# Optimization experiments

Measured on AMD Instinct MI355X. Metric: run time of the kernel, lower is better.

The kernel has to match this reference:

```python
import jax, jax.numpy as jnp
import numpy as np

B, S, D, H = 4, 4096, 256, 4
Dh = D // H


def setup_inputs() -> dict:
    key = jax.random.key(0)
    ks = jax.random.split(key, 5)
    scale = 1.0 / np.sqrt(D)
    return {
        "inputs": jax.random.normal(ks[0], (B, S, D), dtype=jnp.float32),
        "Wq": jax.random.normal(ks[1], (D, D), dtype=jnp.float32) * scale,
        "bq": jnp.zeros((D,), jnp.float32),
        "Wk": jax.random.normal(ks[2], (D, D), dtype=jnp.float32) * scale,
        "bk": jnp.zeros((D,), jnp.float32),
        "Wv": jax.random.normal(ks[3], (D, D), dtype=jnp.float32) * scale,
        "bv": jnp.zeros((D,), jnp.float32),
        "Wo": jax.random.normal(ks[4], (D, D), dtype=jnp.float32) * scale,
        "bo": jnp.zeros((D,), jnp.float32),
    }


def reference(inputs, Wq, bq, Wk, bk, Wv, bv, Wo, bo):
    b, s, d = inputs.shape
    # QKV projections
    q = inputs @ Wq + bq
    k = inputs @ Wk + bk
    v = inputs @ Wv + bv
    # separate heads: [B, S, D] -> [B, H, S, Dh]
    def split_heads(x):
        return x.reshape(b, s, H, Dh).transpose(0, 2, 1, 3)
    q, k, v = split_heads(q), split_heads(k), split_heads(v)
    # scaled dot-product attention (no causal mask: mask=False)
    scores = jnp.einsum("bhqd,bhkd->bhqk", q, k) / jnp.sqrt(jnp.float32(Dh))
    weights = jax.nn.softmax(scores, axis=-1)
    attn = jnp.einsum("bhqk,bhkd->bhqd", weights, v)
    # combine heads: [B, H, S, Dh] -> [B, S, D]
    attn = attn.transpose(0, 2, 1, 3).reshape(b, s, d)
    return attn @ Wo + bo
```

## Files before the change

### kernel.cpp

```cpp
#include <hip/hip_runtime.h>
#include <cmath>

#define B_  4
#define S_  4096
#define D_  256
#define H_  4
#define DH_ 64
#define M_TOTAL (B_*S_)
#define QSCALE 0.1803368801111f

typedef __bf16 bf16x8 __attribute__((ext_vector_type(8)));
typedef __bf16 bf16x4 __attribute__((ext_vector_type(4)));
typedef __bf16 bf16x2 __attribute__((ext_vector_type(2)));
typedef float  f32x4  __attribute__((ext_vector_type(4)));
typedef float  f32x16 __attribute__((ext_vector_type(16)));

#define AS1 __attribute__((address_space(1)))
#define AS3 __attribute__((address_space(3)))

__device__ __forceinline__ void g2lds16(const void* g, void* l) {
    __builtin_amdgcn_global_load_lds((AS1 const void*)g, (AS3 void*)l, 16, 0, 0);
}

#if __has_builtin(__builtin_amdgcn_permlane32_swap)
typedef unsigned uint2v __attribute__((ext_vector_type(2)));
__device__ __forceinline__ void plswap(unsigned &a, unsigned &b) {
    uint2v r = __builtin_amdgcn_permlane32_swap(a, b, false, false);
    a = r[0]; b = r[1];
}
#else
__device__ __forceinline__ void plswap(unsigned &a, unsigned &b) {
    unsigned bl = (unsigned)__shfl_xor((int)b, 32);
    unsigned ah = (unsigned)__shfl_xor((int)a, 32);
    bool hi = (threadIdx.x & 32) != 0;
    unsigned na = hi ? bl : a;
    unsigned nb = hi ? b  : ah;
    a = na; b = nb;
}
#endif

__device__ __forceinline__ unsigned pk2(float x, float y) {
    bf16x2 t; t[0] = (__bf16)x; t[1] = (__bf16)y;
    return __builtin_bit_cast(unsigned, t);
}

__global__ __launch_bounds__(256) void prep(const float* __restrict__ X,
                                            const float* __restrict__ W0,
                                            const float* __restrict__ W1,
                                            const float* __restrict__ W2,
                                            const float* __restrict__ W3,
                                            __bf16* __restrict__ Xb,
                                            __bf16* __restrict__ Wt_all) {
    int t = threadIdx.x;
    if (blockIdx.x < 2048) {
        size_t i = ((size_t)blockIdx.x * 256 + t) * 8;
        float4 v0 = *(const float4*)(X + i);
        float4 v1 = *(const float4*)(X + i + 4);
        bf16x8 o;
        o[0] = (__bf16)v0.x; o[1] = (__bf16)v0.y; o[2] = (__bf16)v0.z; o[3] = (__bf16)v0.w;
        o[4] = (__bf16)v1.x; o[5] = (__bf16)v1.y; o[6] = (__bf16)v1.z; o[7] = (__bf16)v1.w;
        *(bf16x8*)(Xb + i) = o;
        return;
    }
    int bid = blockIdx.x - 2048;
    int z = bid >> 6, rem = bid & 63;
    int by = rem >> 3, bx = rem & 7;
    const float* W = (z == 0) ? W0 : (z == 1) ? W1 : (z == 2) ? W2 : W3;
    float wsc = (z == 0) ? QSCALE : 1.0f;
    __bf16* Wt = Wt_all + (size_t)z * 65536;
    __shared__ float tile[32][33];
    int r0 = by * 32, c0 = bx * 32;
#pragma unroll
    for (int e = 0; e < 4; e++) {
        int idx = t + e * 256; int r = idx >> 5, c = idx & 31;
        tile[r][c] = W[(r0 + r) * 256 + c0 + c];
    }
    __syncthreads();
#pragma unroll
    for (int e = 0; e < 4; e++) {
        int idx = t + e * 256; int r = idx >> 5, c = idx & 31;
        Wt[(c0 + r) * 256 + (r0 + c)] = (__bf16)(tile[c][r] * wsc);
    }
}

__global__ __launch_bounds__(256) void gemm_bt(const __bf16* __restrict__ A,
                                               const __bf16* __restrict__ Wt_all,
                                               const float* __restrict__ bias0,
                                               const float* __restrict__ bias1,
                                               const float* __restrict__ bias2,
                                               __bf16* __restrict__ outb,
                                               __bf16* __restrict__ voutb,
                                               float* __restrict__ outf,
                                               int out_is_f32, float bsc0) {
    constexpr int K = 256;
    __shared__ __attribute__((aligned(16))) __bf16 As[128 * 32];
    __shared__ __attribute__((aligned(16))) __bf16 Bs[128 * 32];

    int t = threadIdx.x;
    int lane = t & 63, w = t >> 6;
    int wr = w >> 1, wc = w & 1;
    int l16 = lane & 15, quad = lane >> 4;
    int mbase = blockIdx.x * 128;
    int nbase = blockIdx.y * 128;
    int z = blockIdx.z;
    const __bf16* Bt = Wt_all + (size_t)z * 65536;
    const float* bias = (z == 0) ? bias0 : (z == 1) ? bias1 : bias2;
    float bscale = (z == 0) ? bsc0 : 1.0f;

    f32x4 acc[4][4] = {};

    int srow = t >> 2;
    int sseg = (t & 3) * 8;

    for (int kk = 0; kk < K; kk += 32) {
        __syncthreads();
        g2lds16(A  + (size_t)(mbase +      srow) * K + kk + sseg, (char*)As +        t * 16);
        g2lds16(A  + (size_t)(mbase + 64 + srow) * K + kk + sseg, (char*)As + 4096 + t * 16);
        g2lds16(Bt + (size_t)(nbase +      srow) * K + kk + sseg, (char*)Bs +        t * 16);
        g2lds16(Bt + (size_t)(nbase + 64 + srow) * K + kk + sseg, (char*)Bs + 4096 + t * 16);
        __syncthreads();

        bf16x8 a[4], b[4];
#pragma unroll
        for (int i = 0; i < 4; i++)
            a[i] = *(const bf16x8*)(As + (wr * 64 + i * 16 + l16) * 32 + quad * 8);
#pragma unroll
        for (int j = 0; j < 4; j++)
            b[j] = *(const bf16x8*)(Bs + (wc * 64 + j * 16 + l16) * 32 + quad * 8);
#pragma unroll
        for (int i = 0; i < 4; i++)
#pragma unroll
            for (int j = 0; j < 4; j++)
                acc[i][j] = __builtin_amdgcn_mfma_f32_16x16x32_bf16(a[i], b[j], acc[i][j], 0, 0, 0);
    }

#pragma unroll
    for (int i = 0; i < 4; i++) {
#pragma unroll
        for (int j = 0; j < 4; j++) {
            int col = nbase + wc * 64 + j * 16 + l16;
            float bv = bias[col] * bscale;
            int row0 = mbase + wr * 64 + i * 16 + quad * 4;
            if (out_is_f32) {
#pragma unroll
                for (int r = 0; r < 4; r++)
                    outf[(size_t)(row0 + r) * 256 + col] = acc[i][j][r] + bv;
            } else if (z == 2) {
                int hcol = col >> 6, dh = col & 63;
                int bidx = row0 >> 12, s0 = row0 & 4095;
                bf16x4 pk;
#pragma unroll
                for (int r = 0; r < 4; r++) pk[r] = (__bf16)(acc[i][j][r] + bv);
                *(bf16x4*)(voutb + ((size_t)(bidx * 4 + hcol) * 64 + dh) * 4096 + s0) = pk;
            } else {
#pragma unroll
                for (int r = 0; r < 4; r++)
                    outb[(size_t)z * ((size_t)M_TOTAL * 256) + (size_t)(row0 + r) * 256 + col] =
                        (__bf16)(acc[i][j][r] + bv);
            }
        }
    }
}

__global__ __launch_bounds__(256, 3) void attn(const __bf16* __restrict__ Qb,
                                               const __bf16* __restrict__ Kb,
                                               const __bf16* __restrict__ Vt,
                                               __bf16* __restrict__ Ctx) {
    __shared__ __attribute__((aligned(16))) __bf16 smem[24576];

    int t = threadIdx.x;
    int lane = t & 63, w = t >> 6;
    int l31 = lane & 31, hh = lane >> 5;
    int kw = w & 1, qw2 = w >> 1;

    int lin = blockIdx.x;
    int xcd = lin & 7, j = lin >> 3;
    int bh = xcd * 2 + (j & 1);
    int qblk = j >> 1;
    int b = bh >> 2, hd = bh & 3;
    int qw = qblk * 128 + qw2 * 64;

    const __bf16* Kbase = Kb + (size_t)b * S_ * 256 + hd * 64;
    const __bf16* Vbase = Vt + (size_t)bh * 64 * S_;

    bf16x8 qf[4][2];
#pragma unroll
    for (int ks = 0; ks < 4; ks++)
#pragma unroll
        for (int qt = 0; qt < 2; qt++)
            qf[ks][qt] = *(const bf16x8*)(Qb + (size_t)(b * S_ + qw + qt * 32 + l31) * 256
                                              + hd * 64 + ks * 16 + hh * 8);

    f32x16 acc[2][2] = {};
    float lsum[2] = {0.f, 0.f};

    int srow = t >> 3;
    int sseg = t & 7;

#define STAGE(kv, slot) do {                                                   \
        char* mk = (char*)smem + (slot) * 16384;                               \
        char* mv = mk + 8192;                                                  \
        _Pragma("unroll")                                                      \
        for (int c = 0; c < 2; c++) {                                          \
            int rr = c * 32 + srow;                                            \
            int gseg = (sseg ^ (rr & 7)) * 8;                                  \
            g2lds16(Kbase + (size_t)((kv) + rr) * 256 + gseg,                  \
                    mk + c * 4096 + t * 16);                                   \
            g2lds16(Vbase + (size_t)rr * S_ + (kv) + gseg,                     \
                    mv + c * 4096 + t * 16);                                   \
        }                                                                      \
    } while (0)

    STAGE(0, 0);
    STAGE(64, 1);

    int rs = 0, ps = 2;
    for (int it = 0; it < 64; it++) {
        if (it < 63) {
            asm volatile("s_waitcnt vmcnt(4)" ::: "memory");
        } else {
            asm volatile("s_waitcnt vmcnt(0)" ::: "memory");
        }
        asm volatile("s_barrier" ::: "memory");
        if (it < 62) STAGE((it + 2) * 64, ps);

        __bf16* Ksp = (__bf16*)((char*)smem + rs * 16384);
        __bf16* Vsp = Ksp + 4096;

        bf16x8 kf[4];
#pragma unroll
        for (int ks = 0; ks < 4; ks++) {
            int slot = (ks * 2 + hh) ^ (l31 & 7);
            kf[ks] = *(const bf16x8*)(Ksp + (kw * 32 + l31) * 64 + slot * 8);
        }
        f32x16 st[2] = {};
#pragma unroll
        for (int ks = 0; ks < 4; ks++)
#pragma unroll
            for (int qt = 0; qt < 2; qt++)
                st[qt] = __builtin_amdgcn_mfma_f32_32x32x16_bf16(kf[ks], qf[ks][qt], st[qt], 0, 0, 0);

        unsigned dd[2][8];
#pragma unroll
        for (int qt = 0; qt < 2; qt++) {
            float p[16];
#pragma unroll
            for (int r = 0; r < 16; r++) p[r] = __builtin_amdgcn_exp2f(st[qt][r]);
            float s0 = ((p[0] + p[1]) + (p[2] + p[3])) + ((p[4] + p[5]) + (p[6] + p[7]));
            float s1 = ((p[8] + p[9]) + (p[10] + p[11])) + ((p[12] + p[13]) + (p[14] + p[15]));
            lsum[qt] += s0 + s1;
#pragma unroll
            for (int m = 0; m < 4; m++) {
                dd[qt][m * 2]     = pk2(p[4 * m],     p[4 * m + 1]);
                dd[qt][m * 2 + 1] = pk2(p[4 * m + 2], p[4 * m + 3]);
            }
        }

#pragma unroll
        for (int tt = 0; tt < 2; tt++) {
            int tks = kw * 2 + tt;
            bf16x8 pf[2];
#pragma unroll
            for (int qt = 0; qt < 2; qt++) {
                unsigned x0 = dd[qt][4 * tt],     y0 = dd[qt][4 * tt + 2];
                unsigned x1 = dd[qt][4 * tt + 1], y1 = dd[qt][4 * tt + 3];
                plswap(x0, y0);
                plswap(x1, y1);
                union { unsigned u[4]; bf16x8 v; } c;
                c.u[0] = x0; c.u[1] = x1; c.u[2] = y0; c.u[3] = y1;
                pf[qt] = c.v;
            }
#pragma unroll
            for (int mt = 0; mt < 2; mt++) {
                int slot = (tks * 2 + hh) ^ (l31 & 7);
                bf16x8 vf = *(const bf16x8*)(Vsp + (mt * 32 + l31) * 64 + slot * 8);
#pragma unroll
                for (int qt = 0; qt < 2; qt++)
                    acc[mt][qt] = __builtin_amdgcn_mfma_f32_32x32x16_bf16(vf, pf[qt], acc[mt][qt], 0, 0, 0);
            }
        }

        rs = (rs == 2) ? 0 : rs + 1;
        ps = (ps == 2) ? 0 : ps + 1;
    }
#undef STAGE

#pragma unroll
    for (int qt = 0; qt < 2; qt++)
        lsum[qt] += __shfl_xor(lsum[qt], 32);

    __syncthreads();
    float* lsd = (float*)((char*)smem + 32768);
    if (kw == 1) {
#pragma unroll
        for (int mt = 0; mt < 2; mt++)
#pragma unroll
            for (int qt = 0; qt < 2; qt++)
#pragma unroll
                for (int g = 0; g < 4; g++) {
                    f32x4 v;
#pragma unroll
                    for (int e = 0; e < 4; e++) v[e] = acc[mt][qt][4 * g + e];
                    *(f32x4*)((char*)smem + qw2 * 16384
                              + ((mt * 2 + qt) * 4 + g) * 1024 + lane * 16) = v;
                }
        lsd[qw2 * 128 + lane * 2 + 0] = lsum[0];
        lsd[qw2 * 128 + lane * 2 + 1] = lsum[1];
    }
    __syncthreads();
    if (kw == 0) {
        float inv[2];
#pragma unroll
        for (int qt = 0; qt < 2; qt++)
            inv[qt] = 1.f / (lsum[qt] + lsd[qw2 * 128 + lane * 2 + qt]);
#pragma unroll
        for (int mt = 0; mt < 2; mt++)
#pragma unroll
            for (int qt = 0; qt < 2; qt++)
#pragma unroll
                for (int g = 0; g < 4; g++) {
                    f32x4 v = *(const f32x4*)((char*)smem + qw2 * 16384
                                              + ((mt * 2 + qt) * 4 + g) * 1024 + lane * 16);
#pragma unroll
                    for (int e = 0; e < 4; e++) acc[mt][qt][4 * g + e] += v[e];
                }
        asm volatile("" ::: "memory");

        __bf16* Es = (__bf16*)((char*)smem + qw2 * 16384);
#pragma unroll
        for (int qt = 0; qt < 2; qt++)
#pragma unroll
            for (int mt = 0; mt < 2; mt++)
#pragma unroll
                for (int rg = 0; rg < 4; rg++) {
                    bf16x4 ov;
#pragma unroll
                    for (int e = 0; e < 4; e++)
                        ov[e] = (__bf16)(acc[mt][qt][4 * rg + e] * inv[qt]);
                    int dhb = mt * 32 + rg * 8 + 4 * hh;
                    *(bf16x4*)(Es + (qt * 32 + l31) * 72 + dhb) = ov;
                }
#pragma unroll
        for (int pass = 0; pass < 8; pass++) {
            int q = pass * 8 + (lane >> 3);
            int col = (lane & 7) * 8;
            bf16x8 val = *(const bf16x8*)(Es + q * 72 + col);
            *(bf16x8*)(Ctx + (size_t)(b * S_ + qw + q) * 256 + hd * 64 + col) = val;
        }
    }
}

extern "C" void kernel_launch(void* const* d_in, const int* in_sizes, int n_in,
                              void* d_out, int out_size, void* d_ws, size_t ws_size,
                              hipStream_t stream) {
    const float* X  = (const float*)d_in[0];
    const float* Wq = (const float*)d_in[1];
    const float* bq = (const float*)d_in[2];
    const float* Wk = (const float*)d_in[3];
    const float* bk = (const float*)d_in[4];
    const float* Wv = (const float*)d_in[5];
    const float* bv = (const float*)d_in[6];
    const float* Wo = (const float*)d_in[7];
    const float* bo = (const float*)d_in[8];
    float* out = (float*)d_out;

    char* ws = (char*)d_ws;
    const size_t MB = 1024 * 1024;
    __bf16* Xb  = (__bf16*)(ws);
    __bf16* Ctx = (__bf16*)(ws);
    __bf16* Wt  = (__bf16*)(ws + 8 * MB);
    __bf16* Qb  = (__bf16*)(ws + 8 * MB + 512 * 1024);
    __bf16* Kb  = (__bf16*)((char*)Qb + 8 * MB);
    __bf16* Vt  = (__bf16*)((char*)Kb + 8 * MB);

    prep<<<dim3(2304), dim3(256), 0, stream>>>(X, Wq, Wk, Wv, Wo, Xb, Wt);
    gemm_bt<<<dim3(M_TOTAL / 128, 2, 3), dim3(256), 0, stream>>>(
        Xb, Wt, bq, bk, bv, Qb, Vt, nullptr, 0, QSCALE);
    attn<<<dim3(512), dim3(256), 0, stream>>>(Qb, Kb, Vt, Ctx);
    gemm_bt<<<dim3(M_TOTAL / 128, 2, 1), dim3(256), 0, stream>>>(
        Ctx, Wt + 3 * 65536, bo, bo, bo, nullptr, nullptr, out, 1, 1.0f);
}
```

Before: 180.3 us.

## Split attention over two KV halves with a separate merge kernel

The attention kernel now splits the key/value sequence into two halves, doubling the grid from 512 to 1024 blocks. Each block writes unnormalized fp32 partial outputs and row sums to workspace. A new merge kernel adds the two partials, normalizes, and writes bf16 context. The aim is better occupancy and load balance on the many-CU GPU, at the cost of an extra launch and roughly 32MB of fp32 partial traffic. The merge appears to rely on the softmax needing no max subtraction, since pre-scaled scores allow plain sums.

```diff
diff --git a/kernel.cpp b/kernel.cpp
--- a/kernel.cpp
+++ b/kernel.cpp
@@ -42,6 +42,12 @@
 __device__ __forceinline__ unsigned pk2(float x, float y) {
     bf16x2 t; t[0] = (__bf16)x; t[1] = (__bf16)y;
     return __builtin_bit_cast(unsigned, t);
+}
+
+__device__ __forceinline__ int part_lin(int bh, int qblk, int ks2) {
+    int xcd = bh >> 1;
+    int j = (ks2 << 6) | (qblk << 1) | (bh & 1);
+    return (j << 3) | xcd;
 }
 
 __global__ __launch_bounds__(256) void prep(const float* __restrict__ X,
@@ -162,10 +168,11 @@
     }
 }
 
-__global__ __launch_bounds__(256, 3) void attn(const __bf16* __restrict__ Qb,
-                                               const __bf16* __restrict__ Kb,
-                                               const __bf16* __restrict__ Vt,
-                                               __bf16* __restrict__ Ctx) {
+__global__ __launch_bounds__(256, 3) void attn_part(const __bf16* __restrict__ Qb,
+                                                    const __bf16* __restrict__ Kb,
+                                                    const __bf16* __restrict__ Vt,
+                                                    float* __restrict__ Opart,
+                                                    float* __restrict__ Lpart) {
     __shared__ __attribute__((aligned(16))) __bf16 smem[24576];
 
     int t = threadIdx.x;
@@ -176,12 +183,13 @@
     int lin = blockIdx.x;
     int xcd = lin & 7, j = lin >> 3;
     int bh = xcd * 2 + (j & 1);
-    int qblk = j >> 1;
+    int qblk = (j >> 1) & 31;
+    int ks2 = j >> 6;
     int b = bh >> 2, hd = bh & 3;
     int qw = qblk * 128 + qw2 * 64;
 
-    const __bf16* Kbase = Kb + (size_t)b * S_ * 256 + hd * 64;
-    const __bf16* Vbase = Vt + (size_t)bh * 64 * S_;
+    const __bf16* Kbase = Kb + (size_t)b * S_ * 256 + hd * 64 + (size_t)ks2 * 2048 * 256;
+    const __bf16* Vbase = Vt + (size_t)bh * 64 * S_ + ks2 * 2048;
 
     bf16x8 qf[4][2];
 #pragma unroll
@@ -215,14 +223,14 @@
     STAGE(64, 1);
 
     int rs = 0, ps = 2;
-    for (int it = 0; it < 64; it++) {
-        if (it < 63) {
+    for (int it = 0; it < 32; it++) {
+        if (it < 31) {
             asm volatile("s_waitcnt vmcnt(4)" ::: "memory");
         } else {
             asm volatile("s_waitcnt vmcnt(0)" ::: "memory");
         }
         asm volatile("s_barrier" ::: "memory");
-        if (it < 62) STAGE((it + 2) * 64, ps);
+        if (it < 30) STAGE((it + 2) * 64, ps);
 
         __bf16* Ksp = (__bf16*)((char*)smem + rs * 16384);
         __bf16* Vsp = Ksp + 4096;
@@ -309,10 +317,11 @@
     }
     __syncthreads();
     if (kw == 0) {
-        float inv[2];
+        float lsc[2];
 #pragma unroll
         for (int qt = 0; qt < 2; qt++)
-            inv[qt] = 1.f / (lsum[qt] + lsd[qw2 * 128 + lane * 2 + qt]);
+            lsc[qt] = lsum[qt] + lsd[qw2 * 128 + lane * 2 + qt];
+        float* Ob = Opart + (size_t)lin * 8192 + qw2 * 4096;
 #pragma unroll
         for (int mt = 0; mt < 2; mt++)
 #pragma unroll
@@ -322,31 +331,74 @@
                     f32x4 v = *(const f32x4*)((char*)smem + qw2 * 16384
                                               + ((mt * 2 + qt) * 4 + g) * 1024 + lane * 16);
 #pragma unroll
-                    for (int e = 0; e < 4; e++) acc[mt][qt][4 * g + e] += v[e];
+                    for (int e = 0; e < 4; e++) v[e] += acc[mt][qt][4 * g + e];
+                    *(f32x4*)(Ob + ((mt * 2 + qt) * 4 + g) * 256 + lane * 4) = v;
                 }
-        asm volatile("" ::: "memory");
-
-        __bf16* Es = (__bf16*)((char*)smem + qw2 * 16384);
+        Lpart[lin * 256 + qw2 * 128 + lane * 2 + 0] = lsc[0];
+        Lpart[lin * 256 + qw2 * 128 + lane * 2 + 1] = lsc[1];
+    }
+}
+
+__global__ __launch_bounds__(256) void attn_merge(const float* __restrict__ Opart,
+                                                  const float* __restrict__ Lpart,
+                                                  __bf16* __restrict__ Ctx) {
+    __shared__ __attribute__((aligned(16))) __bf16 Es_all[4][64 * 72];
+
+    int t = threadIdx.x;
+    int lane = t & 63, w = t >> 6;
+    int l31 = lane & 31, hh = lane >> 5;
+    int id = blockIdx.x * 4 + w;
+    int qw2 = id & 1, qblk = (id >> 1) & 31, bh = id >> 6;
+    int b = bh >> 2, hd = bh & 3;
+    int qw = qblk * 128 + qw2 * 64;
+
+    int lin0 = part_lin(bh, qblk, 0);
+    int lin1 = part_lin(bh, qblk, 1);
+    const float* p0 = Opart + (size_t)lin0 * 8192 + qw2 * 4096;
+    const float* p1 = Opart + (size_t)lin1 * 8192 + qw2 * 4096;
+
+    float inv[2];
+#pragma unroll
+    for (int qt = 0; qt < 2; qt++) {
+        float l0 = Lpart[lin0 * 256 + qw2 * 128 + lane * 2 + qt];
+        float l1 = Lpart[lin1 * 256 + qw2 * 128 + lane * 2 + qt];
+        inv[qt] = 1.f / (l0 + l1);
+    }
+
+    f32x16 acc[2][2];
+#pragma unroll
+    for (int mt = 0; mt < 2; mt++)
 #pragma unroll
         for (int qt = 0; qt < 2; qt++)
 #pragma unroll
-            for (int mt = 0; mt < 2; mt++)
-#pragma unroll
-                for (int rg = 0; rg < 4; rg++) {
-                    bf16x4 ov;
-#pragma unroll
-                    for (int e = 0; e < 4; e++)
-                        ov[e] = (__bf16)(acc[mt][qt][4 * rg + e] * inv[qt]);
-                    int dhb = mt * 32 + rg * 8 + 4 * hh;
-                    *(bf16x4*)(Es + (qt * 32 + l31) * 72 + dhb) = ov;
-                }
-#pragma unroll
-        for (int pass = 0; pass < 8; pass++) {
-            int q = pass * 8 + (lane >> 3);
-            int col = (lane & 7) * 8;
-            bf16x8 val = *(const bf16x8*)(Es + q * 72 + col);
-            *(bf16x8*)(Ctx + (size_t)(b * S_ + qw + q) * 256 + hd * 64 + col) = val;
-        }
+            for (int g = 0; g < 4; g++) {
+                int off = ((mt * 2 + qt) * 4 + g) * 256 + lane * 4;
+                f32x4 v0 = *(const f32x4*)(p0 + off);
+                f32x4 v1 = *(const f32x4*)(p1 + off);
+#pragma unroll
+                for (int e = 0; e < 4; e++) acc[mt][qt][4 * g + e] = v0[e] + v1[e];
+            }
+
+    __bf16* Es = Es_all[w];
+#pragma unroll
+    for (int qt = 0; qt < 2; qt++)
+#pragma unroll
+        for (int mt = 0; mt < 2; mt++)
+#pragma unroll
+            for (int rg = 0; rg < 4; rg++) {
+                bf16x4 ov;
+#pragma unroll
+                for (int e = 0; e < 4; e++)
+                    ov[e] = (__bf16)(acc[mt][qt][4 * rg + e] * inv[qt]);
+                int dhb = mt * 32 + rg * 8 + 4 * hh;
+                *(bf16x4*)(Es + (qt * 32 + l31) * 72 + dhb) = ov;
+            }
+#pragma unroll
+    for (int pass = 0; pass < 8; pass++) {
+        int q = pass * 8 + (lane >> 3);
+        int col = (lane & 7) * 8;
+        bf16x8 val = *(const bf16x8*)(Es + q * 72 + col);
+        *(bf16x8*)(Ctx + (size_t)(b * S_ + qw + q) * 256 + hd * 64 + col) = val;
     }
 }
 
@@ -372,11 +424,14 @@
     __bf16* Qb  = (__bf16*)(ws + 8 * MB + 512 * 1024);
     __bf16* Kb  = (__bf16*)((char*)Qb + 8 * MB);
     __bf16* Vt  = (__bf16*)((char*)Kb + 8 * MB);
+    float*  Opart = (float*)(ws + 33 * MB);
+    float*  Lpart = (float*)(ws + 65 * MB);
 
     prep<<<dim3(2304), dim3(256), 0, stream>>>(X, Wq, Wk, Wv, Wo, Xb, Wt);
     gemm_bt<<<dim3(M_TOTAL / 128, 2, 3), dim3(256), 0, stream>>>(
         Xb, Wt, bq, bk, bv, Qb, Vt, nullptr, 0, QSCALE);
-    attn<<<dim3(512), dim3(256), 0, stream>>>(Qb, Kb, Vt, Ctx);
+    attn_part<<<dim3(1024), dim3(256), 0, stream>>>(Qb, Kb, Vt, Opart, Lpart);
+    attn_merge<<<dim3(256), dim3(256), 0, stream>>>(Opart, Lpart, Ctx);
     gemm_bt<<<dim3(M_TOTAL / 128, 2, 1), dim3(256), 0, stream>>>(
         Ctx, Wt + 3 * 65536, bo, bo, bo, nullptr, nullptr, out, 1, 1.0f);
 }
```

Result: slower. 200.0 us (+10.9%).

## Split attention over key dimension into three partial blocks plus merge kernel

Applied to the files above, without the earlier changes.

Replaces the single attention kernel with a split-K scheme: each block processes one third of the keys (22/21 tiles) for 128 queries, writing fp32 partial outputs and row sums to workspace. A new merge kernel sums the three partials, normalizes, and writes bf16 context. This raises the grid from 512 to 1536 blocks to fill the GPU better and removes the in-block cross-wave LDS reduction. In exchange it adds an extra launch and roughly 48MB of fp32 partial traffic to global memory. Like the original, it relies on exp without max subtraction.

```diff
diff --git a/kernel.cpp b/kernel.cpp
--- a/kernel.cpp
+++ b/kernel.cpp
@@ -42,6 +42,11 @@
 __device__ __forceinline__ unsigned pk2(float x, float y) {
     bf16x2 t; t[0] = (__bf16)x; t[1] = (__bf16)y;
     return __builtin_bit_cast(unsigned, t);
+}
+
+__device__ __forceinline__ int part_lin(int bh, int qblk, int ks3) {
+    int j = (ks3 << 6) | (qblk << 1) | (bh & 1);
+    return (j << 3) | (bh >> 1);
 }
 
 __global__ __launch_bounds__(256) void prep(const float* __restrict__ X,
@@ -162,37 +167,39 @@
     }
 }
 
-__global__ __launch_bounds__(256, 3) void attn(const __bf16* __restrict__ Qb,
-                                               const __bf16* __restrict__ Kb,
-                                               const __bf16* __restrict__ Vt,
-                                               __bf16* __restrict__ Ctx) {
+__global__ __launch_bounds__(256, 3) void attn_part(const __bf16* __restrict__ Qb,
+                                                    const __bf16* __restrict__ Kb,
+                                                    const __bf16* __restrict__ Vt,
+                                                    float* __restrict__ Opart,
+                                                    float* __restrict__ Lpart) {
     __shared__ __attribute__((aligned(16))) __bf16 smem[24576];
 
     int t = threadIdx.x;
     int lane = t & 63, w = t >> 6;
     int l31 = lane & 31, hh = lane >> 5;
-    int kw = w & 1, qw2 = w >> 1;
 
     int lin = blockIdx.x;
     int xcd = lin & 7, j = lin >> 3;
     int bh = xcd * 2 + (j & 1);
-    int qblk = j >> 1;
+    int qblk = (j >> 1) & 31;
+    int ks3 = j >> 6;
     int b = bh >> 2, hd = bh & 3;
-    int qw = qblk * 128 + qw2 * 64;
-
-    const __bf16* Kbase = Kb + (size_t)b * S_ * 256 + hd * 64;
-    const __bf16* Vbase = Vt + (size_t)bh * 64 * S_;
-
-    bf16x8 qf[4][2];
+    int qw = qblk * 128 + w * 32;
+
+    int NT   = ks3 ? 21 : 22;
+    int key0 = ks3 ? (1408 + (ks3 - 1) * 1344) : 0;
+
+    const __bf16* Kbase = Kb + (size_t)b * S_ * 256 + hd * 64 + (size_t)key0 * 256;
+    const __bf16* Vbase = Vt + (size_t)bh * 64 * S_ + key0;
+
+    bf16x8 qf[4];
 #pragma unroll
     for (int ks = 0; ks < 4; ks++)
-#pragma unroll
-        for (int qt = 0; qt < 2; qt++)
-            qf[ks][qt] = *(const bf16x8*)(Qb + (size_t)(b * S_ + qw + qt * 32 + l31) * 256
-                                              + hd * 64 + ks * 16 + hh * 8);
-
-    f32x16 acc[2][2] = {};
-    float lsum[2] = {0.f, 0.f};
+        qf[ks] = *(const bf16x8*)(Qb + (size_t)(b * S_ + qw + l31) * 256
+                                      + hd * 64 + ks * 16 + hh * 8);
+
+    f32x16 acc[2] = {};
+    float lsum = 0.f;
 
     int srow = t >> 3;
     int sseg = t & 7;
@@ -215,138 +222,148 @@
     STAGE(64, 1);
 
     int rs = 0, ps = 2;
-    for (int it = 0; it < 64; it++) {
-        if (it < 63) {
+    for (int it = 0; it < NT; it++) {
+        if (it < NT - 1) {
             asm volatile("s_waitcnt vmcnt(4)" ::: "memory");
         } else {
             asm volatile("s_waitcnt vmcnt(0)" ::: "memory");
         }
         asm volatile("s_barrier" ::: "memory");
-        if (it < 62) STAGE((it + 2) * 64, ps);
+        if (it < NT - 2) STAGE((it + 2) * 64, ps);
 
         __bf16* Ksp = (__bf16*)((char*)smem + rs * 16384);
         __bf16* Vsp = Ksp + 4096;
 
-        bf16x8 kf[4];
-#pragma unroll
-        for (int ks = 0; ks < 4; ks++) {
-            int slot = (ks * 2 + hh) ^ (l31 & 7);
-            kf[ks] = *(const bf16x8*)(Ksp + (kw * 32 + l31) * 64 + slot * 8);
-        }
-        f32x16 st[2] = {};
-#pragma unroll
-        for (int ks = 0; ks < 4; ks++)
-#pragma unroll
-            for (int qt = 0; qt < 2; qt++)
-                st[qt] = __builtin_amdgcn_mfma_f32_32x32x16_bf16(kf[ks], qf[ks][qt], st[qt], 0, 0, 0);
+        f32x16 st[2];
+#pragma unroll
+        for (int kt = 0; kt < 2; kt++) {
+            bf16x8 kf[4];
+#pragma unroll
+            for (int ks = 0; ks < 4; ks++) {
+                int slot = (ks * 2 + hh) ^ (l31 & 7);
+                kf[ks] = *(const bf16x8*)(Ksp + (kt * 32 + l31) * 64 + slot * 8);
+            }
+            st[kt] = (f32x16){};
+#pragma unroll
+            for (int ks = 0; ks < 4; ks++)
+                st[kt] = __builtin_amdgcn_mfma_f32_32x32x16_bf16(kf[ks], qf[ks], st[kt], 0, 0, 0);
+        }
 
         unsigned dd[2][8];
 #pragma unroll
-        for (int qt = 0; qt < 2; qt++) {
+        for (int kt = 0; kt < 2; kt++) {
             float p[16];
 #pragma unroll
-            for (int r = 0; r < 16; r++) p[r] = __builtin_amdgcn_exp2f(st[qt][r]);
+            for (int r = 0; r < 16; r++) p[r] = __builtin_amdgcn_exp2f(st[kt][r]);
             float s0 = ((p[0] + p[1]) + (p[2] + p[3])) + ((p[4] + p[5]) + (p[6] + p[7]));
             float s1 = ((p[8] + p[9]) + (p[10] + p[11])) + ((p[12] + p[13]) + (p[14] + p[15]));
-            lsum[qt] += s0 + s1;
+            lsum += s0 + s1;
 #pragma unroll
             for (int m = 0; m < 4; m++) {
-                dd[qt][m * 2]     = pk2(p[4 * m],     p[4 * m + 1]);
-                dd[qt][m * 2 + 1] = pk2(p[4 * m + 2], p[4 * m + 3]);
+                dd[kt][m * 2]     = pk2(p[4 * m],     p[4 * m + 1]);
+                dd[kt][m * 2 + 1] = pk2(p[4 * m + 2], p[4 * m + 3]);
             }
         }
 
 #pragma unroll
-        for (int tt = 0; tt < 2; tt++) {
-            int tks = kw * 2 + tt;
-            bf16x8 pf[2];
-#pragma unroll
-            for (int qt = 0; qt < 2; qt++) {
-                unsigned x0 = dd[qt][4 * tt],     y0 = dd[qt][4 * tt + 2];
-                unsigned x1 = dd[qt][4 * tt + 1], y1 = dd[qt][4 * tt + 3];
+        for (int kt = 0; kt < 2; kt++)
+#pragma unroll
+            for (int tt = 0; tt < 2; tt++) {
+                int tks = kt * 2 + tt;
+                unsigned x0 = dd[kt][4 * tt],     y0 = dd[kt][4 * tt + 2];
+                unsigned x1 = dd[kt][4 * tt + 1], y1 = dd[kt][4 * tt + 3];
                 plswap(x0, y0);
                 plswap(x1, y1);
                 union { unsigned u[4]; bf16x8 v; } c;
                 c.u[0] = x0; c.u[1] = x1; c.u[2] = y0; c.u[3] = y1;
-                pf[qt] = c.v;
+                bf16x8 pf = c.v;
+#pragma unroll
+                for (int mt = 0; mt < 2; mt++) {
+                    int slot = (tks * 2 + hh) ^ (l31 & 7);
+                    bf16x8 vf = *(const bf16x8*)(Vsp + (mt * 32 + l31) * 64 + slot * 8);
+                    acc[mt] = __builtin_amdgcn_mfma_f32_32x32x16_bf16(vf, pf, acc[mt], 0, 0, 0);
+                }
             }
-#pragma unroll
-            for (int mt = 0; mt < 2; mt++) {
-                int slot = (tks * 2 + hh) ^ (l31 & 7);
-                bf16x8 vf = *(const bf16x8*)(Vsp + (mt * 32 + l31) * 64 + slot * 8);
-#pragma unroll
-                for (int qt = 0; qt < 2; qt++)
-                    acc[mt][qt] = __builtin_amdgcn_mfma_f32_32x32x16_bf16(vf, pf[qt], acc[mt][qt], 0, 0, 0);
-            }
-        }
 
         rs = (rs == 2) ? 0 : rs + 1;
         ps = (ps == 2) ? 0 : ps + 1;
     }
 #undef STAGE
 
-#pragma unroll
-    for (int qt = 0; qt < 2; qt++)
-        lsum[qt] += __shfl_xor(lsum[qt], 32);
-
-    __syncthreads();
-    float* lsd = (float*)((char*)smem + 32768);
-    if (kw == 1) {
-#pragma unroll
-        for (int mt = 0; mt < 2; mt++)
-#pragma unroll
-            for (int qt = 0; qt < 2; qt++)
-#pragma unroll
-                for (int g = 0; g < 4; g++) {
-                    f32x4 v;
-#pragma unroll
-                    for (int e = 0; e < 4; e++) v[e] = acc[mt][qt][4 * g + e];
-                    *(f32x4*)((char*)smem + qw2 * 16384
-                              + ((mt * 2 + qt) * 4 + g) * 1024 + lane * 16) = v;
-                }
-        lsd[qw2 * 128 + lane * 2 + 0] = lsum[0];
-        lsd[qw2 * 128 + lane * 2 + 1] = lsum[1];
-    }
-    __syncthreads();
-    if (kw == 0) {
-        float inv[2];
-#pragma unroll
-        for (int qt = 0; qt < 2; qt++)
-            inv[qt] = 1.f / (lsum[qt] + lsd[qw2 * 128 + lane * 2 + qt]);
-#pragma unroll
-        for (int mt = 0; mt < 2; mt++)
-#pragma unroll
-            for (int qt = 0; qt < 2; qt++)
-#pragma unroll
-                for (int g = 0; g < 4; g++) {
-                    f32x4 v = *(const f32x4*)((char*)smem + qw2 * 16384
-                                              + ((mt * 2 + qt) * 4 + g) * 1024 + lane * 16);
-#pragma unroll
-                    for (int e = 0; e < 4; e++) acc[mt][qt][4 * g + e] += v[e];
-                }
-        asm volatile("" ::: "memory");
-
-        __bf16* Es = (__bf16*)((char*)smem + qw2 * 16384);
-#pragma unroll
-        for (int qt = 0; qt < 2; qt++)
-#pragma unroll
-            for (int mt = 0; mt < 2; mt++)
-#pragma unroll
-                for (int rg = 0; rg < 4; rg++) {
-                    bf16x4 ov;
-#pragma unroll
-                    for (int e = 0; e < 4; e++)
-                        ov[e] = (__bf16)(acc[mt][qt][4 * rg + e] * inv[qt]);
-                    int dhb = mt * 32 + rg * 8 + 4 * hh;
-                    *(bf16x4*)(Es + (qt * 32 + l31) * 72 + dhb) = ov;
-                }
-#pragma unroll
-        for (int pass = 0; pass < 8; pass++) {
-            int q = pass * 8 + (lane >> 3);
-            int col = (lane & 7) * 8;
-            bf16x8 val = *(const bf16x8*)(Es + q * 72 + col);
-            *(bf16x8*)(Ctx + (size_t)(b * S_ + qw + q) * 256 + hd * 64 + col) = val;
-        }
+    lsum += __shfl_xor(lsum, 32);
+
+    float* Ob = Opart + (size_t)lin * 8192 + w * 2048;
+#pragma unroll
+    for (int mt = 0; mt < 2; mt++)
+#pragma unroll
+        for (int g = 0; g < 4; g++) {
+            f32x4 v;
+#pragma unroll
+            for (int e = 0; e < 4; e++) v[e] = acc[mt][4 * g + e];
+            *(f32x4*)(Ob + (mt * 4 + g) * 256 + lane * 4) = v;
+        }
+    if (hh == 0)
+        Lpart[lin * 128 + w * 32 + l31] = lsum;
+}
+
+__global__ __launch_bounds__(256) void attn_merge(const float* __restrict__ Opart,
+                                                  const float* __restrict__ Lpart,
+                                                  __bf16* __restrict__ Ctx) {
+    __shared__ __attribute__((aligned(16))) __bf16 Es_all[4][32 * 72];
+
+    int t = threadIdx.x;
+    int lane = t & 63, w = t >> 6;
+    int l31 = lane & 31, hh = lane >> 5;
+    int id = blockIdx.x * 4 + w;
+    int ws = id & 3;
+    int qblk = (id >> 2) & 31;
+    int bh = id >> 7;
+    int b = bh >> 2, hd = bh & 3;
+    int qw = qblk * 128 + ws * 32;
+
+    int lin0 = part_lin(bh, qblk, 0);
+    int lin1 = part_lin(bh, qblk, 1);
+    int lin2 = part_lin(bh, qblk, 2);
+    const float* p0 = Opart + (size_t)lin0 * 8192 + ws * 2048;
+    const float* p1 = Opart + (size_t)lin1 * 8192 + ws * 2048;
+    const float* p2 = Opart + (size_t)lin2 * 8192 + ws * 2048;
+
+    float l0 = Lpart[lin0 * 128 + ws * 32 + l31];
+    float l1 = Lpart[lin1 * 128 + ws * 32 + l31];
+    float l2 = Lpart[lin2 * 128 + ws * 32 + l31];
+    float inv = 1.f / (l0 + l1 + l2);
+
+    f32x16 acc[2];
+#pragma unroll
+    for (int mt = 0; mt < 2; mt++)
+#pragma unroll
+        for (int g = 0; g < 4; g++) {
+            int off = (mt * 4 + g) * 256 + lane * 4;
+            f32x4 v0 = *(const f32x4*)(p0 + off);
+            f32x4 v1 = *(const f32x4*)(p1 + off);
+            f32x4 v2 = *(const f32x4*)(p2 + off);
+#pragma unroll
+            for (int e = 0; e < 4; e++) acc[mt][4 * g + e] = v0[e] + v1[e] + v2[e];
+        }
+
+    __bf16* Es = Es_all[w];
+#pragma unroll
+    for (int mt = 0; mt < 2; mt++)
+#pragma unroll
+        for (int g = 0; g < 4; g++) {
+            bf16x4 ov;
+#pragma unroll
+            for (int e = 0; e < 4; e++)
+                ov[e] = (__bf16)(acc[mt][4 * g + e] * inv);
+            int dhb = mt * 32 + g * 8 + 4 * hh;
+            *(bf16x4*)(Es + l31 * 72 + dhb) = ov;
+        }
+#pragma unroll
+    for (int pass = 0; pass < 4; pass++) {
+        int q = pass * 8 + (lane >> 3);
+        int col = (lane & 7) * 8;
+        bf16x8 val = *(const bf16x8*)(Es + q * 72 + col);
+        *(bf16x8*)(Ctx + (size_t)(b * S_ + qw + q) * 256 + hd * 64 + col) = val;
     }
 }
 
@@ -372,11 +389,14 @@
     __bf16* Qb  = (__bf16*)(ws + 8 * MB + 512 * 1024);
     __bf16* Kb  = (__bf16*)((char*)Qb + 8 * MB);
     __bf16* Vt  = (__bf16*)((char*)Kb + 8 * MB);
+    float*  Opart = (float*)(ws + 33 * MB);
+    float*  Lpart = (float*)(ws + 81 * MB);
 
     prep<<<dim3(2304), dim3(256), 0, stream>>>(X, Wq, Wk, Wv, Wo, Xb, Wt);
     gemm_bt<<<dim3(M_TOTAL / 128, 2, 3), dim3(256), 0, stream>>>(
         Xb, Wt, bq, bk, bv, Qb, Vt, nullptr, 0, QSCALE);
-    attn<<<dim3(512), dim3(256), 0, stream>>>(Qb, Kb, Vt, Ctx);
+    attn_part<<<dim3(1536), dim3(256), 0, stream>>>(Qb, Kb, Vt, Opart, Lpart);
+    attn_merge<<<dim3(512), dim3(256), 0, stream>>>(Opart, Lpart, Ctx);
     gemm_bt<<<dim3(M_TOTAL / 128, 2, 1), dim3(256), 0, stream>>>(
         Ctx, Wt + 3 * 65536, bo, bo, bo, nullptr, nullptr, out, 1, 1.0f);
 }
```

After: 187.6 us. +4.0%, slower.
